# Performance work log

Measured on AMD Instinct MI355X. Metric: run time of the kernel, lower is better.

## Reference

```python
import jax, jax.numpy as jnp
import numpy as np

B, F, D = 512, 128, 1024
EPS = 1e-5

def _ln(x, g, b):
    mu = jnp.mean(x, axis=-1, keepdims=True)
    var = jnp.mean(jnp.square(x - mu), axis=-1, keepdims=True)
    return (x - mu) * jax.lax.rsqrt(var + EPS) * g + b

def setup_inputs() -> dict:
    key = jax.random.key(0)
    ks = jax.random.split(key, 8)
    inp = {
        "text_embeds": jax.random.normal(ks[0], (B, D), jnp.float32),
        "video_embeds": jax.random.normal(ks[1], (B, F, D), jnp.float32),
    }
    # Linear weights: torch init is eye for all proj/linear layers; use small random
    # perturbation of identity to keep math non-trivial but realistic.
    def w(k):
        return jnp.eye(D, dtype=jnp.float32) + 0.02 * jax.random.normal(k, (D, D), jnp.float32)
    inp["q_w"], inp["k_w"], inp["v_w"] = w(ks[2]), w(ks[3]), w(ks[4])
    inp["out_w"], inp["lin_w"] = w(ks[5]), w(ks[6])
    for n in ("q_b", "k_b", "v_b", "out_b", "lin_b"):
        inp[n] = jnp.zeros((D,), jnp.float32)
    for i in (1, 2, 3):
        inp[f"ln{i}_g"] = jnp.ones((D,), jnp.float32)
        inp[f"ln{i}_b"] = jnp.zeros((D,), jnp.float32)
    return inp

def reference(text_embeds, video_embeds, q_w, k_w, v_w, out_w, lin_w,
              q_b, k_b, v_b, out_b, lin_b,
              ln1_g, ln1_b, ln2_g, ln2_b, ln3_g, ln3_b):
    t = _ln(text_embeds, ln1_g, ln1_b)                 # [B, D]
    vf = _ln(video_embeds, ln1_g, ln1_b)               # [B, F, D]
    q = t @ q_w.T + q_b                                # [B, D]
    k = vf @ k_w.T + k_b                               # [B, F, D]
    v = vf @ v_w.T + v_b                               # [B, F, D]
    logits = jnp.einsum("bd,bfd->bf", q, k) / jnp.sqrt(jnp.float32(D))
    w_att = jax.nn.softmax(logits, axis=-1)            # [B, F]
    attn = jnp.einsum("bf,bfd->bd", w_att, v)          # [B, D]
    attn = attn @ out_w.T + out_b
    attn_out = _ln(attn, ln2_g, ln2_b)
    linear_out = attn_out @ lin_w.T + lin_b
    # dropout: eval mode (identity)
    out = attn_out + linear_out
    return _ln(out, ln3_g, ln3_b)
```

## Files before the change

### kernel.cpp

```cpp
#include <hip/hip_runtime.h>

#define B_ 512
#define F_ 128
#define D_ 1024
#define EPS_ 1e-5f

typedef float f32x4 __attribute__((ext_vector_type(4)));
typedef __bf16 bf16x4 __attribute__((ext_vector_type(4)));
typedef __bf16 bf16x8 __attribute__((ext_vector_type(8)));

template <int OUT>
__global__ __launch_bounds__(256) void k_ln(
    const float* __restrict__ X, const float* __restrict__ g,
    const float* __restrict__ bv, float* __restrict__ Yf,
    __bf16* __restrict__ Yh, __bf16* __restrict__ Yl) {
  int row = blockIdx.x, t = threadIdx.x;
  f32x4 xv = *(const f32x4*)(X + (size_t)row * D_ + t * 4);
  float s = xv[0] + xv[1] + xv[2] + xv[3];
  float ss = xv[0] * xv[0] + xv[1] * xv[1] + xv[2] * xv[2] + xv[3] * xv[3];
#pragma unroll
  for (int o = 32; o > 0; o >>= 1) { s += __shfl_xor(s, o); ss += __shfl_xor(ss, o); }
  __shared__ float ws[4][2];
  int w = t >> 6;
  if ((t & 63) == 0) { ws[w][0] = s; ws[w][1] = ss; }
  __syncthreads();
  s = ws[0][0] + ws[1][0] + ws[2][0] + ws[3][0];
  ss = ws[0][1] + ws[1][1] + ws[2][1] + ws[3][1];
  float mu = s * (1.0f / D_);
  float var = ss * (1.0f / D_) - mu * mu;
  float rs = rsqrtf(var + EPS_);
  f32x4 gg = *(const f32x4*)(g + t * 4);
  f32x4 bb = *(const f32x4*)(bv + t * 4);
  f32x4 o4;
#pragma unroll
  for (int i = 0; i < 4; i++) o4[i] = (xv[i] - mu) * rs * gg[i] + bb[i];
  if (OUT == 0) {
    *(f32x4*)(Yf + (size_t)row * D_ + t * 4) = o4;
  } else {
    bf16x4 h4, l4;
#pragma unroll
    for (int i = 0; i < 4; i++) {
      h4[i] = (__bf16)o4[i];
      l4[i] = (__bf16)(o4[i] - (float)h4[i]);
    }
    *(bf16x4*)(Yh + (size_t)row * D_ + t * 4) = h4;
    *(bf16x4*)(Yl + (size_t)row * D_ + t * 4) = l4;
  }
}

__global__ __launch_bounds__(256) void k_final(
    const __bf16* __restrict__ X1h, const __bf16* __restrict__ X1l,
    const float* __restrict__ X2, const float* __restrict__ g,
    const float* __restrict__ bv, float* __restrict__ out) {
  int row = blockIdx.x, t = threadIdx.x;
  bf16x4 h4 = *(const bf16x4*)(X1h + (size_t)row * D_ + t * 4);
  bf16x4 l4 = *(const bf16x4*)(X1l + (size_t)row * D_ + t * 4);
  f32x4 b = *(const f32x4*)(X2 + (size_t)row * D_ + t * 4);
  f32x4 v;
#pragma unroll
  for (int i = 0; i < 4; i++) v[i] = (float)h4[i] + (float)l4[i] + b[i];
  float s = v[0] + v[1] + v[2] + v[3];
  float ss = v[0] * v[0] + v[1] * v[1] + v[2] * v[2] + v[3] * v[3];
#pragma unroll
  for (int o = 32; o > 0; o >>= 1) { s += __shfl_xor(s, o); ss += __shfl_xor(ss, o); }
  __shared__ float ws[4][2];
  int w = t >> 6;
  if ((t & 63) == 0) { ws[w][0] = s; ws[w][1] = ss; }
  __syncthreads();
  s = ws[0][0] + ws[1][0] + ws[2][0] + ws[3][0];
  ss = ws[0][1] + ws[1][1] + ws[2][1] + ws[3][1];
  float mu = s * (1.0f / D_);
  float var = ss * (1.0f / D_) - mu * mu;
  float rs = rsqrtf(var + EPS_);
  f32x4 gg = *(const f32x4*)(g + t * 4);
  f32x4 bb = *(const f32x4*)(bv + t * 4);
  f32x4 o4;
#pragma unroll
  for (int i = 0; i < 4; i++) o4[i] = (v[i] - mu) * rs * gg[i] + bb[i];
  *(f32x4*)(out + (size_t)row * D_ + t * 4) = o4;
}

__global__ __launch_bounds__(256) void k_wprep(
    const float* __restrict__ w0, const float* __restrict__ w1,
    const float* __restrict__ w2, const float* __restrict__ w3,
    const float* __restrict__ w4, __bf16* __restrict__ o0,
    __bf16* __restrict__ o1, __bf16* __restrict__ o2,
    __bf16* __restrict__ o3, __bf16* __restrict__ o4p) {
  int z = blockIdx.z;
  const float* src = (z == 0) ? w0 : (z == 1) ? w1 : (z == 2) ? w2 : (z == 3) ? w3 : w4;
  __bf16* dst = (z == 0) ? o0 : (z == 1) ? o1 : (z == 2) ? o2 : (z == 3) ? o3 : o4p;
  int t = threadIdx.x;
  if (z != 1) {
    int row = blockIdx.y * 32 + (t >> 3);
    int col = blockIdx.x * 32 + (t & 7) * 4;
    f32x4 v = *(const f32x4*)(src + (size_t)row * D_ + col);
    bf16x4 o;
    o[0] = (__bf16)v[0]; o[1] = (__bf16)v[1]; o[2] = (__bf16)v[2]; o[3] = (__bf16)v[3];
    *(bf16x4*)(dst + (size_t)row * D_ + col) = o;
  } else {
    __shared__ float tile[32][33];
    int ti = blockIdx.y, tj = blockIdx.x;
    int c = t & 31, r0 = t >> 5;
#pragma unroll
    for (int i = 0; i < 4; i++) {
      int r = r0 + i * 8;
      tile[r][c] = src[(size_t)(ti * 32 + r) * D_ + tj * 32 + c];
    }
    __syncthreads();
#pragma unroll
    for (int i = 0; i < 4; i++) {
      int r = r0 + i * 8;
      dst[(size_t)(tj * 32 + r) * D_ + ti * 32 + c] = (__bf16)tile[c][r];
    }
  }
}

template <int OUT>
__global__ __launch_bounds__(512) void k_gemm32(
    const __bf16* __restrict__ Ah, const __bf16* __restrict__ Al,
    const __bf16* __restrict__ W, const float* __restrict__ bias,
    float* __restrict__ Cf, __bf16* __restrict__ Ch, __bf16* __restrict__ Cl,
    int N, int K) {
  int t = threadIdx.x;
  int lane = t & 63, wv = t >> 6;
  int r = lane & 15, quad = lane >> 4;
  int tn = blockIdx.x, tm = blockIdx.y;
  int kw = K >> 3;
  const __bf16* pah0 = Ah + (size_t)(tm * 32 + r) * K + wv * kw + quad * 8;
  const __bf16* pah1 = pah0 + (size_t)16 * K;
  const __bf16* pal0 = Al + (size_t)(tm * 32 + r) * K + wv * kw + quad * 8;
  const __bf16* pal1 = pal0 + (size_t)16 * K;
  const __bf16* pw0 = W + (size_t)(tn * 32 + r) * K + wv * kw + quad * 8;
  const __bf16* pw1 = pw0 + (size_t)16 * K;
  f32x4 acc00 = {0,0,0,0}, acc01 = {0,0,0,0}, acc10 = {0,0,0,0}, acc11 = {0,0,0,0};
  bf16x8 ah0 = *(const bf16x8*)pah0, ah1 = *(const bf16x8*)pah1;
  bf16x8 al0 = *(const bf16x8*)pal0, al1 = *(const bf16x8*)pal1;
  bf16x8 w0v = *(const bf16x8*)pw0, w1v = *(const bf16x8*)pw1;
  for (int k0 = 0; k0 < kw; k0 += 32) {
    int kn = (k0 + 32 < kw) ? (k0 + 32) : 0;
    bf16x8 nah0 = *(const bf16x8*)(pah0 + kn);
    bf16x8 nah1 = *(const bf16x8*)(pah1 + kn);
    bf16x8 nal0 = *(const bf16x8*)(pal0 + kn);
    bf16x8 nal1 = *(const bf16x8*)(pal1 + kn);
    bf16x8 nw0 = *(const bf16x8*)(pw0 + kn);
    bf16x8 nw1 = *(const bf16x8*)(pw1 + kn);
    acc00 = __builtin_amdgcn_mfma_f32_16x16x32_bf16(ah0, w0v, acc00, 0, 0, 0);
    acc01 = __builtin_amdgcn_mfma_f32_16x16x32_bf16(ah0, w1v, acc01, 0, 0, 0);
    acc10 = __builtin_amdgcn_mfma_f32_16x16x32_bf16(ah1, w0v, acc10, 0, 0, 0);
    acc11 = __builtin_amdgcn_mfma_f32_16x16x32_bf16(ah1, w1v, acc11, 0, 0, 0);
    acc00 = __builtin_amdgcn_mfma_f32_16x16x32_bf16(al0, w0v, acc00, 0, 0, 0);
    acc01 = __builtin_amdgcn_mfma_f32_16x16x32_bf16(al0, w1v, acc01, 0, 0, 0);
    acc10 = __builtin_amdgcn_mfma_f32_16x16x32_bf16(al1, w0v, acc10, 0, 0, 0);
    acc11 = __builtin_amdgcn_mfma_f32_16x16x32_bf16(al1, w1v, acc11, 0, 0, 0);
    ah0 = nah0; ah1 = nah1; al0 = nal0; al1 = nal1; w0v = nw0; w1v = nw1;
  }
  __shared__ float red[8][64][17];
  *(f32x4*)(&red[wv][lane][0])  = acc00;
  *(f32x4*)(&red[wv][lane][4])  = acc01;
  *(f32x4*)(&red[wv][lane][8])  = acc10;
  *(f32x4*)(&red[wv][lane][12]) = acc11;
  __syncthreads();
  int re = lane & 15, qe = lane >> 4;
#pragma unroll
  for (int u = 0; u < 2; u++) {
    int j = (t >> 6) * 2 + u;
    int a = j >> 2, i = j & 3;
    float val = 0.0f;
#pragma unroll
    for (int ww = 0; ww < 8; ww++) val += red[ww][lane][j];
    int row = tm * 32 + qe * 4 + i + ((a >> 1) << 4);
    int col = tn * 32 + re + ((a & 1) << 4);
    if (bias) val += bias[col];
    size_t o = (size_t)row * N + col;
    if (OUT == 0) {
      Cf[o] = val;
    } else {
      __bf16 h = (__bf16)val;
      Ch[o] = h;
      Cl[o] = (__bf16)(val - (float)h);
    }
  }
}

__global__ __launch_bounds__(256) void k_prep_q(
    const float* __restrict__ q2, const __bf16* __restrict__ qh,
    const __bf16* __restrict__ ql, const float* __restrict__ g,
    const float* __restrict__ bv, const float* __restrict__ kb,
    float* __restrict__ gq, float* __restrict__ sum_gq,
    float* __restrict__ dot_bq, float* __restrict__ qkb) {
  int b = blockIdx.x, t = threadIdx.x;
  f32x4 q2v = *(const f32x4*)(q2 + (size_t)b * D_ + t * 4);
  bf16x4 h4 = *(const bf16x4*)(qh + (size_t)b * D_ + t * 4);
  bf16x4 l4 = *(const bf16x4*)(ql + (size_t)b * D_ + t * 4);
  f32x4 gg = *(const f32x4*)(g + t * 4);
  f32x4 bb = *(const f32x4*)(bv + t * 4);
  f32x4 kk = *(const f32x4*)(kb + t * 4);
  f32x4 gqv;
  float s1 = 0.f, s2 = 0.f, s3 = 0.f;
#pragma unroll
  for (int i = 0; i < 4; i++) {
    gqv[i] = gg[i] * q2v[i];
    s1 += gqv[i];
    s2 += bb[i] * q2v[i];
    s3 += kk[i] * ((float)h4[i] + (float)l4[i]);
  }
  *(f32x4*)(gq + (size_t)b * D_ + t * 4) = gqv;
#pragma unroll
  for (int o = 32; o > 0; o >>= 1) {
    s1 += __shfl_xor(s1, o); s2 += __shfl_xor(s2, o); s3 += __shfl_xor(s3, o);
  }
  __shared__ float ws[4][3];
  int w = t >> 6;
  if ((t & 63) == 0) { ws[w][0] = s1; ws[w][1] = s2; ws[w][2] = s3; }
  __syncthreads();
  if (t == 0) {
    sum_gq[b] = ws[0][0] + ws[1][0] + ws[2][0] + ws[3][0];
    dot_bq[b] = ws[0][1] + ws[1][1] + ws[2][1] + ws[3][1];
    qkb[b] = ws[0][2] + ws[1][2] + ws[2][2] + ws[3][2];
  }
}

#define XPAD 1032
__global__ __launch_bounds__(1024) void k_attn(
    const float* __restrict__ video, const float* __restrict__ gq,
    const float* __restrict__ sum_gq, const float* __restrict__ dot_bq,
    const float* __restrict__ qkb, const float* __restrict__ g,
    const float* __restrict__ bv, __bf16* __restrict__ ctxh,
    __bf16* __restrict__ ctxl) {
  __shared__ float X[32][XPAD];
  __shared__ float l_s[32], mu_s[32], rs_s[32], a_s[32];
  __shared__ float alpha_s, S_s, C_s;
  int b = blockIdx.x, t = threadIdx.x;
  int row = t >> 5, c = t & 31;
  const float* vbase = video + ((size_t)b * F_ + row) * D_ + c * 4;
  f32x4 gqr[8];
  const float* gp = gq + (size_t)b * D_ + c * 4;
#pragma unroll
  for (int i = 0; i < 8; i++) gqr[i] = *(const f32x4*)(gp + i * 128);
  float sgq = sum_gq[b], dbq = dot_bq[b], qk = qkb[b];
  f32x4 vr[8];
#pragma unroll
  for (int i = 0; i < 8; i++) vr[i] = *(const f32x4*)(vbase + i * 128);
  float O = 0.0f;
  float m_run = -1e30f, S = 0.0f, Cc = 0.0f;
  for (int T = 0; T < 4; T++) {
    float sx = 0.f, sxx = 0.f, sxg = 0.f;
#pragma unroll
    for (int i = 0; i < 8; i++) {
      f32x4 v = vr[i];
      sx += v[0] + v[1] + v[2] + v[3];
      sxx += v[0]*v[0] + v[1]*v[1] + v[2]*v[2] + v[3]*v[3];
      f32x4 gg = gqr[i];
      sxg += v[0]*gg[0] + v[1]*gg[1] + v[2]*gg[2] + v[3]*gg[3];
      *(f32x4*)(&X[row][c * 4 + i * 128]) = v;
    }
#pragma unroll
    for (int o = 16; o > 0; o >>= 1) {
      sx += __shfl_xor(sx, o);
      sxx += __shfl_xor(sxx, o);
      sxg += __shfl_xor(sxg, o);
    }
    if (c == 0) {
      float mu = sx * (1.0f / D_);
      float var = sxx * (1.0f / D_) - mu * mu;
      float rs = rsqrtf(var + EPS_);
      l_s[row] = (rs * (sxg - mu * sgq) + dbq + qk) * 0.03125f;
      mu_s[row] = mu; rs_s[row] = rs;
    }
    if (T < 3) {
      const float* nb = vbase + (size_t)(T + 1) * 32 * D_;
#pragma unroll
      for (int i = 0; i < 8; i++) vr[i] = *(const f32x4*)(nb + i * 128);
    }
    __syncthreads();
    if (t < 32) {
      float lf = l_s[t], mt = lf;
#pragma unroll
      for (int o = 16; o > 0; o >>= 1) mt = fmaxf(mt, __shfl_xor(mt, o));
      float m_new = fmaxf(m_run, mt);
      float alpha = __expf(m_run - m_new);
      float e = __expf(lf - m_new);
      float af = e * rs_s[t];
      a_s[t] = af;
      float se = e, sc = af * mu_s[t];
#pragma unroll
      for (int o = 16; o > 0; o >>= 1) {
        se += __shfl_xor(se, o);
        sc += __shfl_xor(sc, o);
      }
      S = S * alpha + se;
      Cc = Cc * alpha + sc;
      m_run = m_new;
      if (t == 0) { alpha_s = alpha; S_s = S; C_s = Cc; }
    }
    __syncthreads();
    float alpha = alpha_s;
    float acc = 0.0f;
#pragma unroll
    for (int fi = 0; fi < 32; fi++) acc += a_s[fi] * X[fi][t];
    O = O * alpha + acc;
    if (T < 3) __syncthreads();
  }
  float inv = 1.0f / S_s;
  float v = g[t] * ((O - C_s) * inv) + bv[t];
  __bf16 h = (__bf16)v;
  ctxh[(size_t)b * D_ + t] = h;
  ctxl[(size_t)b * D_ + t] = (__bf16)(v - (float)h);
}

extern "C" void kernel_launch(void* const* d_in, const int* in_sizes, int n_in,
                              void* d_out, int out_size, void* d_ws, size_t ws_size,
                              hipStream_t stream) {
  (void)in_sizes; (void)n_in; (void)out_size; (void)ws_size;
  const float* text = (const float*)d_in[0];
  const float* video = (const float*)d_in[1];
  const float* q_w = (const float*)d_in[2];
  const float* k_w = (const float*)d_in[3];
  const float* v_w = (const float*)d_in[4];
  const float* out_w = (const float*)d_in[5];
  const float* lin_w = (const float*)d_in[6];
  const float* q_b = (const float*)d_in[7];
  const float* k_b = (const float*)d_in[8];
  const float* v_b = (const float*)d_in[9];
  const float* out_b = (const float*)d_in[10];
  const float* lin_b = (const float*)d_in[11];
  const float* ln1_g = (const float*)d_in[12];
  const float* ln1_b = (const float*)d_in[13];
  const float* ln2_g = (const float*)d_in[14];
  const float* ln2_b = (const float*)d_in[15];
  const float* ln3_g = (const float*)d_in[16];
  const float* ln3_b = (const float*)d_in[17];
  float* out = (float*)d_out;

  const size_t BD = (size_t)B_ * D_;
  const size_t DD = (size_t)D_ * D_;
  float* f = (float*)d_ws;
  float* slotF1 = f;
  float* slotF2 = f + BD;
  float* sum_gq = f + 2 * BD;
  float* dot_bq = sum_gq + B_;
  float* qkb = sum_gq + 2 * B_;
  __bf16* P1h = (__bf16*)(sum_gq + 4 * B_);
  __bf16* P1l = P1h + BD;
  __bf16* P2h = P1h + 2 * BD;
  __bf16* P2l = P1h + 3 * BD;
  __bf16* P3h = P1h + 4 * BD;
  __bf16* P3l = P1h + 5 * BD;
  __bf16* Wq = P1h + 6 * BD;
  __bf16* WkT = Wq + DD;
  __bf16* Wv = Wq + 2 * DD;
  __bf16* Wo = Wq + 3 * DD;
  __bf16* Wl = Wq + 4 * DD;

  dim3 gemm_grid(D_ / 32, B_ / 32);

  k_wprep<<<dim3(32, 32, 5), 256, 0, stream>>>(q_w, k_w, v_w, out_w, lin_w,
                                               Wq, WkT, Wv, Wo, Wl);
  k_ln<1><<<B_, 256, 0, stream>>>(text, ln1_g, ln1_b, nullptr, P1h, P1l);
  k_gemm32<1><<<gemm_grid, 512, 0, stream>>>(P1h, P1l, Wq, q_b, nullptr, P2h, P2l, D_, D_);
  k_gemm32<0><<<gemm_grid, 512, 0, stream>>>(P2h, P2l, WkT, nullptr, slotF1, nullptr, nullptr, D_, D_);
  k_prep_q<<<B_, 256, 0, stream>>>(slotF1, P2h, P2l, ln1_g, ln1_b, k_b,
                                   slotF2, sum_gq, dot_bq, qkb);
  k_attn<<<B_, 1024, 0, stream>>>(video, slotF2, sum_gq, dot_bq, qkb,
                                  ln1_g, ln1_b, P1h, P1l);
  k_gemm32<1><<<gemm_grid, 512, 0, stream>>>(P1h, P1l, Wv, v_b, nullptr, P2h, P2l, D_, D_);
  k_gemm32<0><<<gemm_grid, 512, 0, stream>>>(P2h, P2l, Wo, out_b, slotF1, nullptr, nullptr, D_, D_);
  k_ln<1><<<B_, 256, 0, stream>>>(slotF1, ln2_g, ln2_b, nullptr, P3h, P3l);
  k_gemm32<0><<<gemm_grid, 512, 0, stream>>>(P3h, P3l, Wl, lin_b, slotF2, nullptr, nullptr, D_, D_);
  k_final<<<B_, 256, 0, stream>>>(P3h, P3l, slotF2, ln3_g, ln3_b, out);
}
```

Before: 505.3 us.

## Restructure attention kernel as per-wave online softmax with final cross-wave merge

Each of the 16 waves now owns 8 frames and runs its own online softmax and accumulation in registers, one frame at a time, with a one-frame register prefetch. This replaces the old loop that staged 32-frame tiles in shared memory and needed several block-wide barriers per tile. The per-wave max, sum and correction terms are merged once at the end through a small shared buffer and a cross-wave reduction. Per-thread register use grows because each thread holds 16 output accumulators plus two frame buffers, which may lower occupancy.

```diff
diff --git a/kernel.cpp b/kernel.cpp
--- a/kernel.cpp
+++ b/kernel.cpp
@@ -220,89 +220,97 @@
   }
 }
 
-#define XPAD 1032
 __global__ __launch_bounds__(1024) void k_attn(
     const float* __restrict__ video, const float* __restrict__ gq,
     const float* __restrict__ sum_gq, const float* __restrict__ dot_bq,
     const float* __restrict__ qkb, const float* __restrict__ g,
     const float* __restrict__ bv, __bf16* __restrict__ ctxh,
     __bf16* __restrict__ ctxl) {
-  __shared__ float X[32][XPAD];
-  __shared__ float l_s[32], mu_s[32], rs_s[32], a_s[32];
-  __shared__ float alpha_s, S_s, C_s;
+  __shared__ float Xc[16][1032];
+  __shared__ float mSC[16][4];
   int b = blockIdx.x, t = threadIdx.x;
-  int row = t >> 5, c = t & 31;
-  const float* vbase = video + ((size_t)b * F_ + row) * D_ + c * 4;
-  f32x4 gqr[8];
-  const float* gp = gq + (size_t)b * D_ + c * 4;
-#pragma unroll
-  for (int i = 0; i < 8; i++) gqr[i] = *(const f32x4*)(gp + i * 128);
+  int w = t >> 6, lane = t & 63;
+  f32x4 gqr[4];
+  const float* gp = gq + (size_t)b * D_ + lane * 4;
+#pragma unroll
+  for (int i = 0; i < 4; i++) gqr[i] = *(const f32x4*)(gp + i * 256);
   float sgq = sum_gq[b], dbq = dot_bq[b], qk = qkb[b];
-  f32x4 vr[8];
-#pragma unroll
-  for (int i = 0; i < 8; i++) vr[i] = *(const f32x4*)(vbase + i * 128);
-  float O = 0.0f;
+  const float* vbase = video + ((size_t)b * F_ + w * 8) * D_ + lane * 4;
+  f32x4 vA[4], vB[4];
+#pragma unroll
+  for (int i = 0; i < 4; i++) vA[i] = *(const f32x4*)(vbase + i * 256);
+  f32x4 O[4];
+#pragma unroll
+  for (int i = 0; i < 4; i++) O[i] = (f32x4){0.f, 0.f, 0.f, 0.f};
   float m_run = -1e30f, S = 0.0f, Cc = 0.0f;
-  for (int T = 0; T < 4; T++) {
+  for (int f = 0; f < 8; f++) {
+    if (f < 7) {
+      const float* nb = vbase + (size_t)(f + 1) * D_;
+#pragma unroll
+      for (int i = 0; i < 4; i++) vB[i] = *(const f32x4*)(nb + i * 256);
+    }
     float sx = 0.f, sxx = 0.f, sxg = 0.f;
 #pragma unroll
-    for (int i = 0; i < 8; i++) {
-      f32x4 v = vr[i];
-      sx += v[0] + v[1] + v[2] + v[3];
-      sxx += v[0]*v[0] + v[1]*v[1] + v[2]*v[2] + v[3]*v[3];
-      f32x4 gg = gqr[i];
-      sxg += v[0]*gg[0] + v[1]*gg[1] + v[2]*gg[2] + v[3]*gg[3];
-      *(f32x4*)(&X[row][c * 4 + i * 128]) = v;
-    }
-#pragma unroll
-    for (int o = 16; o > 0; o >>= 1) {
+    for (int i = 0; i < 4; i++) {
+      f32x4 v = vA[i], gg = gqr[i];
+#pragma unroll
+      for (int j = 0; j < 4; j++) {
+        sx += v[j];
+        sxx += v[j] * v[j];
+        sxg += v[j] * gg[j];
+      }
+    }
+#pragma unroll
+    for (int o = 32; o > 0; o >>= 1) {
       sx += __shfl_xor(sx, o);
       sxx += __shfl_xor(sxx, o);
       sxg += __shfl_xor(sxg, o);
     }
-    if (c == 0) {
-      float mu = sx * (1.0f / D_);
-      float var = sxx * (1.0f / D_) - mu * mu;
-      float rs = rsqrtf(var + EPS_);
-      l_s[row] = (rs * (sxg - mu * sgq) + dbq + qk) * 0.03125f;
-      mu_s[row] = mu; rs_s[row] = rs;
-    }
-    if (T < 3) {
-      const float* nb = vbase + (size_t)(T + 1) * 32 * D_;
-#pragma unroll
-      for (int i = 0; i < 8; i++) vr[i] = *(const f32x4*)(nb + i * 128);
-    }
-    __syncthreads();
-    if (t < 32) {
-      float lf = l_s[t], mt = lf;
-#pragma unroll
-      for (int o = 16; o > 0; o >>= 1) mt = fmaxf(mt, __shfl_xor(mt, o));
-      float m_new = fmaxf(m_run, mt);
-      float alpha = __expf(m_run - m_new);
-      float e = __expf(lf - m_new);
-      float af = e * rs_s[t];
-      a_s[t] = af;
-      float se = e, sc = af * mu_s[t];
-#pragma unroll
-      for (int o = 16; o > 0; o >>= 1) {
-        se += __shfl_xor(se, o);
-        sc += __shfl_xor(sc, o);
-      }
-      S = S * alpha + se;
-      Cc = Cc * alpha + sc;
-      m_run = m_new;
-      if (t == 0) { alpha_s = alpha; S_s = S; C_s = Cc; }
-    }
-    __syncthreads();
-    float alpha = alpha_s;
-    float acc = 0.0f;
-#pragma unroll
-    for (int fi = 0; fi < 32; fi++) acc += a_s[fi] * X[fi][t];
-    O = O * alpha + acc;
-    if (T < 3) __syncthreads();
-  }
-  float inv = 1.0f / S_s;
-  float v = g[t] * ((O - C_s) * inv) + bv[t];
+    float mu = sx * (1.0f / D_);
+    float var = sxx * (1.0f / D_) - mu * mu;
+    float rs = rsqrtf(var + EPS_);
+    float l = (rs * (sxg - mu * sgq) + dbq + qk) * 0.03125f;
+    float m_new = fmaxf(m_run, l);
+    float alpha = __expf(m_run - m_new);
+    float e = __expf(l - m_new);
+    float af = e * rs;
+    S = S * alpha + e;
+    Cc = Cc * alpha + af * mu;
+#pragma unroll
+    for (int i = 0; i < 4; i++) {
+#pragma unroll
+      for (int j = 0; j < 4; j++) O[i][j] = O[i][j] * alpha + af * vA[i][j];
+    }
+    m_run = m_new;
+#pragma unroll
+    for (int i = 0; i < 4; i++) vA[i] = vB[i];
+  }
+  if (lane == 0) { mSC[w][0] = m_run; mSC[w][1] = S; mSC[w][2] = Cc; }
+  __syncthreads();
+  float mstar = -1e30f;
+#pragma unroll
+  for (int i = 0; i < 16; i++) mstar = fmaxf(mstar, mSC[i][0]);
+  float myscale = __expf(m_run - mstar);
+#pragma unroll
+  for (int i = 0; i < 4; i++) {
+    f32x4 o4;
+#pragma unroll
+    for (int j = 0; j < 4; j++) o4[j] = O[i][j] * myscale;
+    *(f32x4*)(&Xc[w][lane * 4 + i * 256]) = o4;
+  }
+  float Sstar = 0.f, Cstar = 0.f;
+#pragma unroll
+  for (int i = 0; i < 16; i++) {
+    float e = __expf(mSC[i][0] - mstar);
+    Sstar += mSC[i][1] * e;
+    Cstar += mSC[i][2] * e;
+  }
+  __syncthreads();
+  float Osum = 0.f;
+#pragma unroll
+  for (int i = 0; i < 16; i++) Osum += Xc[i][t];
+  float inv = 1.0f / Sstar;
+  float v = g[t] * ((Osum - Cstar) * inv) + bv[t];
   __bf16 h = (__bf16)v;
   ctxh[(size_t)b * D_ + t] = h;
   ctxl[(size_t)b * D_ + t] = (__bf16)(v - (float)h);
```

After: 485.9 us. 3.8% less time.
